# Performance work log

Measured on AMD Instinct MI355X. Metric: run time of the kernel, lower is better.

The kernel has to match this reference:

```python
import jax, jax.numpy as jnp
import numpy as np

M, L, P, KK = 8, 3, 12, 9  # n_heads, n_levels, n_points, patch_size**2

def lrelu(v):
    return jnp.where(v >= 0, v, 0.1 * v)

def conv2d(x, w, b, pad):
    y = jax.lax.conv_general_dilated(x, w, (1, 1), [(pad, pad), (pad, pad)], dimension_numbers=('NCHW', 'OIHW', 'NCHW'))
    return y + b[None, :, None, None]

def trunk(x, w1, b1, w2, b2, w3, b3, w4, b4):
    h = lrelu(conv2d(x, w1, b1, 0))
    h = lrelu(conv2d(h, w2, b2, 1))
    h = lrelu(conv2d(h, w3, b3, 1))
    return conv2d(h, w4, b4, 0)

def grid_sample(img, gx, gy, align_corners):
    # img [N,C,H,W]; gx,gy [N,Q] normalized to [-1,1]; bilinear, zeros padding
    N, C, H, W = img.shape
    if align_corners:
        ix = (gx + 1.0) * 0.5 * (W - 1)
        iy = (gy + 1.0) * 0.5 * (H - 1)
    else:
        ix = ((gx + 1.0) * W - 1.0) * 0.5
        iy = ((gy + 1.0) * H - 1.0) * 0.5
    ix0 = jnp.floor(ix); iy0 = jnp.floor(iy)
    wx1 = ix - ix0; wy1 = iy - iy0
    flat = img.reshape(N, C, H * W)
    def gather(xi, yi, wgt):
        valid = (xi >= 0) & (xi <= W - 1) & (yi >= 0) & (yi <= H - 1)
        idx = (jnp.clip(yi, 0, H - 1) * W + jnp.clip(xi, 0, W - 1)).astype(jnp.int32)
        v = jnp.take_along_axis(flat, idx[:, None, :], axis=2)
        return v * (wgt * valid)[:, None, :]
    return (gather(ix0, iy0, (1 - wx1) * (1 - wy1)) + gather(ix0 + 1, iy0, wx1 * (1 - wy1))
            + gather(ix0, iy0 + 1, (1 - wx1) * wy1) + gather(ix0 + 1, iy0 + 1, wx1 * wy1))

def flow_warp(img, flow):
    # img [n,c,h,w]; flow [n,2,h,w] in pixels; torch grid_sample align_corners=True, zeros padding
    n, c, h, w = img.shape
    gy, gx = jnp.meshgrid(jnp.arange(h, dtype=img.dtype), jnp.arange(w, dtype=img.dtype), indexing='ij')
    gxn = 2.0 * (gx[None] + flow[:, 0]) / max(w - 1, 1) - 1.0
    gyn = 2.0 * (gy[None] + flow[:, 1]) / max(h - 1, 1) - 1.0
    return grid_sample(img, gxn.reshape(n, -1), gyn.reshape(n, -1), True).reshape(n, c, h, w)

def msdeform_attn(value, loc, attn, h, w):
    # pytorch MSDeformAttn core: value [N,L*HW,M,D]; loc [N,HW,M,L,Pt,2]; attn [N,HW,M,L,Pt]
    N, _, _, D = value.shape
    HW = h * w
    Pt = loc.shape[4]
    grids = 2.0 * loc - 1.0
    sampled = []
    for l in range(L):
        v = value[:, l * HW:(l + 1) * HW].transpose(0, 2, 3, 1).reshape(N * M, D, h, w)
        g = grids[:, :, :, l].transpose(0, 2, 1, 3, 4).reshape(N * M, HW * Pt, 2)
        s = grid_sample(v, g[..., 0], g[..., 1], False)  # [N*M, D, HW*Pt]
        sampled.append(s.reshape(N * M, D, HW, Pt))
    sampled = jnp.concatenate(sampled, axis=-1)  # [N*M, D, HW, L*Pt]
    aw = attn.transpose(0, 2, 1, 3, 4).reshape(N * M, HW, L * Pt)
    out = jnp.einsum('ndqp,nqp->nqd', sampled, aw)
    return out.reshape(N, M, HW, D).transpose(0, 2, 1, 3).reshape(N, HW, M * D)

def _forward(x, flow_1, flow_2, flip_flow_1, flip_flow_2, aw_w1, aw_b1, aw_w2, aw_b2, aw_w3, aw_b3, aw_w4, aw_b4, so_w1, so_b1, so_w2, so_b2, so_w3, so_b3, so_w4, so_b4, po_w1, po_b1, po_w2, po_b2, po_w3, po_b3, po_w4, po_b4, vp_w, vp_b, op_w1, op_b1, op_w2, op_b2):
    n, t, c, h, w = x.shape
    HW = h * w
    flow_cn1 = flow_1
    flow_cn2 = flow_1 + flow_warp(flow_2, flow_cn1)
    warp1 = flow_warp(x[:, 1], flow_cn1)
    warp2 = flow_warp(x[:, 2], flow_cn2)
    extra = jnp.concatenate([x[:, 0], warp1, warp2, flow_cn1, flow_cn2], axis=1)  # [n, 3c+4, h, w]
    value = conv2d(x.reshape(n, t * c, h, w), vp_w, vp_b, 0)
    off = trunk(extra, so_w1, so_b1, so_w2, so_b2, so_w3, so_b3, so_w4, so_b4)
    aw = trunk(extra, aw_w1, aw_b1, aw_w2, aw_b2, aw_w3, aw_b3, aw_w4, aw_b4)
    po = trunk(extra, po_w1, po_b1, po_w2, po_b2, po_w3, po_b3, po_w4, po_b4)
    value = value.reshape(n, t, c, HW).transpose(0, 1, 3, 2).reshape(n, t * HW, M, c // M)
    off = off.reshape(n, -1, HW).transpose(0, 2, 1).reshape(n, HW, M, L, P, 2)
    po = po.reshape(n, -1, HW).transpose(0, 2, 1).reshape(n, HW, M, L, P)
    po = jax.nn.sigmoid(po) * 3.0
    aw = aw.reshape(n, -1, HW).transpose(0, 2, 1).reshape(n, HW, M, L * P * KK)
    aw = jax.nn.softmax(aw, axis=-1).reshape(n, HW, M, L, P * KK)
    # flow-guided per-level offsets: level0 zeros, level1 flow_cn1, level2 flow_cn2
    f1 = flow_cn1.reshape(n, 2, HW).transpose(0, 2, 1)
    f2 = flow_cn2.reshape(n, 2, HW).transpose(0, 2, 1)
    fstack = jnp.stack([jnp.zeros_like(f1), f1, f2], axis=2)  # [n,HW,L,2]
    off = off + fstack[:, :, None, :, None, :]
    # 3x3 patch around each sampling point, scaled by learned patch offsets
    a = jnp.arange(-1, 2, dtype=x.dtype)
    pnx, pny = jnp.meshgrid(a, a, indexing='ij')
    p_n = jnp.stack([pnx, pny], axis=-1).reshape(KK, 2)
    off = off[..., None, :] + p_n * po[..., None, None]  # [n,HW,M,L,P,KK,2]
    off = off.reshape(n, HW, M, L, P * KK, 2)
    # reference points (valid ratios == 1)
    ry = (jnp.arange(h, dtype=x.dtype) + 0.5) / h
    rx = (jnp.arange(w, dtype=x.dtype) + 0.5) / w
    gy, gx = jnp.meshgrid(ry, rx, indexing='ij')
    ref = jnp.stack([gx, gy], axis=-1).reshape(1, HW, 1, 1, 1, 2)
    norm = jnp.array([w, h], dtype=x.dtype)
    loc = ref + off / norm
    out = msdeform_attn(value, loc, aw, h, w)  # [n, HW, c]
    feat = out.reshape(n, h, w, c).transpose(0, 3, 1, 2)
    res = conv2d(lrelu(conv2d(feat, op_w1, op_b1, 0)), op_w2, op_b2, 0)
    return res + x[:, 0]

def setup_inputs():
    key = jax.random.key(0)
    keys = jax.random.split(key, 64)
    it = iter(range(64))
    def nrm(shape, scale):
        return jax.random.normal(keys[next(it)], shape, jnp.float32) * scale
    n, t, c, h, w = 1, 3, 64, 64, 64
    Cin = t * c + 4  # 196
    d = {}
    d['x'] = nrm((n, t, c, h, w), 1.0)
    for nm in ['flow_1', 'flow_2', 'flip_flow_1', 'flip_flow_2']:
        d[nm] = nrm((n, 2, h, w), 1.5)
    def branch(prefix, out_ch, final_scale):
        d[prefix + '_w1'] = nrm((64, Cin, 1, 1), 1.0 / np.sqrt(Cin))
        d[prefix + '_b1'] = nrm((64,), 0.01)
        d[prefix + '_w2'] = nrm((64, 64, 3, 3), 1.0 / np.sqrt(64 * 9))
        d[prefix + '_b2'] = nrm((64,), 0.01)
        d[prefix + '_w3'] = nrm((64, 64, 3, 3), 1.0 / np.sqrt(64 * 9))
        d[prefix + '_b3'] = nrm((64,), 0.01)
        d[prefix + '_w4'] = nrm((out_ch, 64, 1, 1), final_scale)
        d[prefix + '_b4'] = nrm((out_ch,), 0.01)
    branch('aw', M * L * P * KK, 0.01)
    branch('so', M * L * P * 2, 0.01)
    branch('po', M * L * P, 0.01)
    d['vp_w'] = nrm((t * c, t * c, 1, 1), 1.0 / np.sqrt(t * c))
    d['vp_b'] = nrm((t * c,), 0.01)
    d['op_w1'] = nrm((c, c, 1, 1), 1.0 / np.sqrt(c))
    d['op_b1'] = nrm((c,), 0.01)
    d['op_w2'] = nrm((c, c, 1, 1), 1.0 / np.sqrt(c))
    d['op_b2'] = nrm((c,), 0.01)
    return d

def reference(x, flow_1, flow_2, flip_flow_1, flip_flow_2, aw_w1, aw_b1, aw_w2, aw_b2, aw_w3, aw_b3, aw_w4, aw_b4, so_w1, so_b1, so_w2, so_b2, so_w3, so_b3, so_w4, so_b4, po_w1, po_b1, po_w2, po_b2, po_w3, po_b3, po_w4, po_b4, vp_w, vp_b, op_w1, op_b1, op_w2, op_b2):
    return _forward(x, flow_1, flow_2, flip_flow_1, flip_flow_2, aw_w1, aw_b1, aw_w2, aw_b2, aw_w3, aw_b3, aw_w4, aw_b4, so_w1, so_b1, so_w2, so_b2, so_w3, so_b3, so_w4, so_b4, po_w1, po_b1, po_w2, po_b2, po_w3, po_b3, po_w4, po_b4, vp_w, vp_b, op_w1, op_b1, op_w2, op_b2)
```

## Files before the change

kernel.cpp:

```cpp
#include <hip/hip_runtime.h>
#include <hip/hip_bf16.h>
#include <math.h>

#define HWN 4096

typedef __attribute__((ext_vector_type(8))) short short8;
typedef __attribute__((ext_vector_type(4))) float f32x4;

__device__ __forceinline__ float lrelu_f(float v) { return v >= 0.f ? v : 0.1f * v; }

__device__ __forceinline__ unsigned short f2bf(float f) {
  union { float f; unsigned u; } v; v.f = f;
  unsigned r = v.u + 0x7fff + ((v.u >> 16) & 1);
  return (unsigned short)(r >> 16);
}
__device__ __forceinline__ float bf2f(unsigned short u) {
  union { unsigned u; float f; } v; v.u = ((unsigned)u) << 16;
  return v.f;
}
__device__ __forceinline__ float bf_lo(unsigned u) {
  union { unsigned u; float f; } v; v.u = u << 16; return v.f;
}
__device__ __forceinline__ float bf_hi(unsigned u) {
  union { unsigned u; float f; } v; v.u = u & 0xffff0000u; return v.f;
}

__device__ __forceinline__ float bilin_zero(const float* __restrict__ img, float ix, float iy) {
  float fx0 = floorf(ix), fy0 = floorf(iy);
  int x0 = (int)fx0, y0 = (int)fy0;
  float wx1 = ix - fx0, wy1 = iy - fy0;
  float wx0 = 1.f - wx1, wy0 = 1.f - wy1;
  float acc = 0.f;
  if ((unsigned)y0 < 64u) {
    if ((unsigned)x0 < 64u)       acc += wx0 * wy0 * img[y0 * 64 + x0];
    if ((unsigned)(x0 + 1) < 64u) acc += wx1 * wy0 * img[y0 * 64 + x0 + 1];
  }
  if ((unsigned)(y0 + 1) < 64u) {
    if ((unsigned)x0 < 64u)       acc += wx0 * wy1 * img[(y0 + 1) * 64 + x0];
    if ((unsigned)(x0 + 1) < 64u) acc += wx1 * wy1 * img[(y0 + 1) * 64 + x0 + 1];
  }
  return acc;
}

__global__ void k_pre(
    const float* __restrict__ x, const float* __restrict__ flow1, const float* __restrict__ flow2,
    const float* so_w4, const float* po_w4, const float* aw_w4,
    const float* so_b4, const float* po_b4, const float* aw_b4,
    const float* so_b1, const float* po_b1, const float* aw_b1,
    const float* so_b2, const float* po_b2, const float* aw_b2,
    const float* so_b3, const float* po_b3, const float* aw_b3,
    const float* so_w1, const float* po_w1, const float* aw_w1,
    const float* so_w2, const float* po_w2, const float* aw_w2,
    const float* so_w3, const float* po_w3, const float* aw_w3,
    const float* op_w1, const float* op_w2, const float* vp_w,
    unsigned short* Wtail, float* btail, float* b1c, float* b2c, float* b3c,
    unsigned short* o1b, unsigned short* o2b, unsigned short* W1,
    unsigned short* W2g, unsigned short* W3g, unsigned short* vpb,
    unsigned short* xb, float* fcn2) {
  __shared__ unsigned short tile[64 * 65];
  int gx = blockIdx.x;
  int tid = threadIdx.x;
  if (gx < 5184) {
    int y = gx / 864;
    int t = (gx % 864) * 256 + tid;
    if (y == 0) {
      if (t < 3456 * 64) {
        int row = t >> 6, k = t & 63;
        float v = row < 576 ? so_w4[row * 64 + k]
                : row < 864 ? po_w4[(row - 576) * 64 + k]
                            : aw_w4[(row - 864) * 64 + k];
        Wtail[t] = f2bf(v);
      }
    } else if (y == 1) {
      if (t < 3456) {
        btail[t] = t < 576 ? so_b4[t] : t < 864 ? po_b4[t - 576] : aw_b4[t - 864];
      } else if (t < 3648) {
        int i = t - 3456; b1c[i] = i < 64 ? so_b1[i] : i < 128 ? po_b1[i - 64] : aw_b1[i - 128];
      } else if (t < 3840) {
        int i = t - 3648; b2c[i] = i < 64 ? so_b2[i] : i < 128 ? po_b2[i - 64] : aw_b2[i - 128];
      } else if (t < 4032) {
        int i = t - 3840; b3c[i] = i < 64 ? so_b3[i] : i < 128 ? po_b3[i - 64] : aw_b3[i - 128];
      } else if (t < 8128) {
        o1b[t - 4032] = f2bf(op_w1[t - 4032]);
      } else if (t < 12224) {
        o2b[t - 8128] = f2bf(op_w2[t - 8128]);
      }
    } else if (y == 2) {
      if (t < 192 * 224) {
        int row = t / 224, k = t % 224;
        int tr = row >> 6, lco = row & 63;
        const float* s = tr == 0 ? so_w1 : tr == 1 ? po_w1 : aw_w1;
        W1[t] = (k < 196) ? f2bf(s[lco * 196 + k]) : (unsigned short)0;
      }
    } else if (y == 3 || y == 4) {
      if (t < 3 * 64 * 576) {
        int tr = t / 36864, rem = t % 36864;
        int co = rem / 576, r2 = rem % 576;
        int kidx = r2 >> 6, ci = r2 & 63;
        const float* s;
        if (y == 3) s = tr == 0 ? so_w2 : tr == 1 ? po_w2 : aw_w2;
        else        s = tr == 0 ? so_w3 : tr == 1 ? po_w3 : aw_w3;
        (y == 3 ? W2g : W3g)[t] = f2bf(s[co * 576 + ci * 9 + kidx]);
      }
    } else {
      if (t < 192 * 192) vpb[t] = f2bf(vp_w[t]);
    }
  } else if (gx < 5376) {
    int b = gx - 5184;
    int ptile = b & 63, cg = b >> 6;
    int px = tid & 63, ch0 = (tid >> 6) * 16;
#pragma unroll
    for (int i = 0; i < 16; i++) {
      float v = x[(size_t)(cg * 64 + ch0 + i) * HWN + ptile * 64 + px];
      tile[(ch0 + i) * 65 + px] = f2bf(v);
    }
    __syncthreads();
    int c = tid & 63, pl0 = (tid >> 6) * 16;
#pragma unroll
    for (int i = 0; i < 16; i++)
      xb[(size_t)(ptile * 64 + pl0 + i) * 192 + cg * 64 + c] = tile[c * 65 + pl0 + i];
  } else {
    int p = (gx - 5376) * 256 + tid;
    int px = p & 63, py = p >> 6;
    float fx = flow1[p], fy = flow1[HWN + p];
    float ix = (float)px + fx, iy = (float)py + fy;
    fcn2[p] = fx + bilin_zero(flow2, ix, iy);
    fcn2[HWN + p] = fy + bilin_zero(flow2 + HWN, ix, iy);
  }
}

__global__ void k_extra(const unsigned short* __restrict__ xb, const float* __restrict__ flow1,
                        const float* __restrict__ fcn2, unsigned short* __restrict__ extra) {
  int w = threadIdx.x >> 6, c = threadIdx.x & 63;
  int p = blockIdx.x * 4 + w;
  int px = p & 63, py = p >> 6;
  float fx1 = flow1[p], fy1 = flow1[HWN + p];
  float fx2 = fcn2[p],  fy2 = fcn2[HWN + p];
  extra[(size_t)p * 224 + c] = xb[(size_t)p * 192 + c];
#pragma unroll
  for (int lev = 0; lev < 2; lev++) {
    float ix = (float)px + (lev ? fx2 : fx1);
    float iy = (float)py + (lev ? fy2 : fy1);
    float fx0 = floorf(ix), fy0 = floorf(iy);
    int x0 = (int)fx0, y0 = (int)fy0;
    float wx1 = ix - fx0, wy1 = iy - fy0;
    float wx0 = 1.f - wx1, wy0 = 1.f - wy1;
    int coff = (lev + 1) * 64;
    float acc = 0.f;
    if ((unsigned)y0 < 64u) {
      if ((unsigned)x0 < 64u)       acc += wx0 * wy0 * bf2f(xb[(size_t)(y0 * 64 + x0) * 192 + coff + c]);
      if ((unsigned)(x0 + 1) < 64u) acc += wx1 * wy0 * bf2f(xb[(size_t)(y0 * 64 + x0 + 1) * 192 + coff + c]);
    }
    if ((unsigned)(y0 + 1) < 64u) {
      if ((unsigned)x0 < 64u)       acc += wx0 * wy1 * bf2f(xb[(size_t)((y0 + 1) * 64 + x0) * 192 + coff + c]);
      if ((unsigned)(x0 + 1) < 64u) acc += wx1 * wy1 * bf2f(xb[(size_t)((y0 + 1) * 64 + x0 + 1) * 192 + coff + c]);
    }
    extra[(size_t)p * 224 + coff + c] = f2bf(acc);
  }
  if (c < 2) {
    extra[(size_t)p * 224 + 192 + c] = f2bf(flow1[c * HWN + p]);
    extra[(size_t)p * 224 + 194 + c] = f2bf(fcn2[c * HWN + p]);
  }
  if (c < 28) extra[(size_t)p * 224 + 196 + c] = 0;
}

__global__ __launch_bounds__(128) void k_gemm2(
    const unsigned short* __restrict__ A0, const unsigned short* __restrict__ Wm0,
    const float* __restrict__ bias0, unsigned short* __restrict__ out0,
    const unsigned short* __restrict__ A1, const unsigned short* __restrict__ Wm1,
    const float* __restrict__ bias1, unsigned short* __restrict__ out1) {
  int z = blockIdx.z;
  const unsigned short* A = z ? A1 : A0;
  const unsigned short* Wm = z ? Wm1 : Wm0;
  const float* bias = z ? bias1 : bias0;
  unsigned short* out = z ? out1 : out0;
  int K = z ? 224 : 192;

  int wv = threadIdx.x >> 6;
  int l = threadIdx.x & 63;
  int lm = l & 15, lq = l >> 4;
  int p0 = blockIdx.x * 32 + wv * 16;
  int co0 = blockIdx.y * 32;

  f32x4 acc[2];
#pragma unroll
  for (int nt = 0; nt < 2; nt++) {
    float bv = bias[co0 + nt * 16 + lm];
    acc[nt] = (f32x4){bv, bv, bv, bv};
  }
  const unsigned short* ap = A + (size_t)(p0 + lm) * K + lq * 8;
  const unsigned short* wp = Wm + (size_t)(co0 + lm) * K + lq * 8;
  for (int k0 = 0; k0 < K; k0 += 32) {
    short8 af = *(const short8*)(ap + k0);
#pragma unroll
    for (int nt = 0; nt < 2; nt++) {
      short8 bf = *(const short8*)(wp + (size_t)nt * 16 * K + k0);
      acc[nt] = __builtin_amdgcn_mfma_f32_16x16x32_bf16(af, bf, acc[nt], 0, 0, 0);
    }
  }
#pragma unroll
  for (int nt = 0; nt < 2; nt++) {
    int co = co0 + nt * 16 + lm;
#pragma unroll
    for (int r = 0; r < 4; r++) {
      int p = p0 + lq * 4 + r;
      float v = acc[nt][r];
      if (z) v = lrelu_f(v);
      out[(size_t)p * 192 + co] = f2bf(v);
    }
  }
}

__global__ __launch_bounds__(128) void k_conv3g(const unsigned short* __restrict__ h,
                                                const unsigned short* __restrict__ Wm,
                                                const float* __restrict__ bias,
                                                unsigned short* __restrict__ out) {
  int wv = threadIdx.x >> 6;
  int l = threadIdx.x & 63;
  int lm = l & 15, lq = l >> 4;
  int p0 = blockIdx.x * 32 + wv * 16;
  int co0 = blockIdx.y * 16;
  int t = blockIdx.z;
  int p = p0 + lm;
  int px = p & 63, py = p >> 6;

  float bv = bias[t * 64 + co0 + lm];
  f32x4 acc = (f32x4){bv, bv, bv, bv};
  const unsigned short* wp = Wm + ((size_t)t * 64 + co0 + lm) * 576 + lq * 8;
#pragma unroll
  for (int kidx = 0; kidx < 9; kidx++) {
    int ky = kidx / 3, kx = kidx % 3;
    int pp = p + (ky - 1) * 64 + (kx - 1);
    bool valid = ((unsigned)(px + kx - 1) < 64u) && ((unsigned)(py + ky - 1) < 64u);
    const unsigned short* apb = h + (size_t)pp * 192 + t * 64 + lq * 8;
#pragma unroll
    for (int c2 = 0; c2 < 2; c2++) {
      short8 af = {};
      if (valid) af = *(const short8*)(apb + c2 * 32);
      short8 bf = *(const short8*)(wp + kidx * 64 + c2 * 32);
      acc = __builtin_amdgcn_mfma_f32_16x16x32_bf16(af, bf, acc, 0, 0, 0);
    }
  }
#pragma unroll
  for (int r = 0; r < 4; r++) {
    int po_ = p0 + lq * 4 + r;
    out[(size_t)po_ * 192 + t * 64 + co0 + lm] = f2bf(lrelu_f(acc[r]));
  }
}

__global__ __launch_bounds__(256) void k_tail(const unsigned short* __restrict__ A,
                                              const unsigned short* __restrict__ Wm,
                                              const float* __restrict__ bias,
                                              unsigned short* __restrict__ out) {
  int wv = threadIdx.x >> 6;
  int l = threadIdx.x & 63;
  int lm = l & 15, lq = l >> 4;
  int p0 = blockIdx.x * 64 + wv * 16;
  int co0 = blockIdx.y * 32;
  int t = (co0 < 576) ? 0 : (co0 < 864 ? 1 : 2);

  f32x4 acc[2];
#pragma unroll
  for (int nt = 0; nt < 2; nt++) {
    float bv = bias[co0 + nt * 16 + lm];
    acc[nt] = (f32x4){bv, bv, bv, bv};
  }
  const unsigned short* ap = A + (size_t)(p0 + lm) * 192 + t * 64 + lq * 8;
  const unsigned short* wp = Wm + (size_t)(co0 + lm) * 64 + lq * 8;
#pragma unroll
  for (int k0 = 0; k0 < 64; k0 += 32) {
    short8 af = *(const short8*)(ap + k0);
#pragma unroll
    for (int nt = 0; nt < 2; nt++) {
      short8 bf = *(const short8*)(wp + (size_t)nt * 16 * 64 + k0);
      acc[nt] = __builtin_amdgcn_mfma_f32_16x16x32_bf16(af, bf, acc[nt], 0, 0, 0);
    }
  }
#pragma unroll
  for (int nt = 0; nt < 2; nt++) {
    int co = co0 + nt * 16 + lm;
#pragma unroll
    for (int r = 0; r < 4; r++) {
      int p = p0 + lq * 4 + r;
      float v = acc[nt][r];
      if (t == 2) v = __expf(v);
      else if (t == 1) v = 3.f * __builtin_amdgcn_rcpf(1.f + __expf(-v));
      out[(size_t)p * 3456 + co] = f2bf(v);
    }
  }
}

__global__ void k_msdeform(const unsigned short* __restrict__ vsb,
                           const unsigned short* __restrict__ to,
                           const float* __restrict__ flow1, const float* __restrict__ fcn2,
                           unsigned short* __restrict__ featb) {
  int yl = threadIdx.x & 15;
  int p = blockIdx.x * 16 + (threadIdx.x >> 4);
  int m = blockIdx.y;
  int px = p & 63, py = p >> 6;

  float fx1 = flow1[p], fy1 = flow1[HWN + p];
  float fx2 = fcn2[p],  fy2 = fcn2[HWN + p];

  const unsigned short* row = to + (size_t)p * 3456;

  float acc[8];
#pragma unroll
  for (int d = 0; d < 8; d++) acc[d] = 0.f;
  float wsum = 0.f;

  for (int pair = yl; pair < 36; pair += 16) {
    int l = pair / 12, pt = pair % 12;
    float fx = (l == 1) ? fx1 : ((l == 2) ? fx2 : 0.f);
    float fy = (l == 1) ? fy1 : ((l == 2) ? fy2 : 0.f);
    int ch = (m * 3 + l) * 12 + pt;
    unsigned ow = *(const unsigned*)(row + ch * 2);
    float ox = bf_lo(ow);
    float oy = bf_hi(ow);
    float s = bf2f(row[576 + ch]);
    float bx = (float)px + ox + fx;
    float by = (float)py + oy + fy;
    const unsigned short* vbase = vsb + l * 64 + m * 8;
    const unsigned short* lgp = row + 864 + m * 324 + l * 108 + pt * 9;
#pragma unroll
    for (int kk = 0; kk < 9; kk++) {
      float pnx = (float)(kk / 3 - 1);
      float pny = (float)(kk % 3 - 1);
      float ix = bx + pnx * s;
      float iy = by + pny * s;
      float wgt = bf2f(lgp[kk]);
      wsum += wgt;

      float fx0 = floorf(ix), fy0 = floorf(iy);
      int x0 = (int)fx0, y0 = (int)fy0;
      float wx1 = ix - fx0, wy1 = iy - fy0;
      float wx0 = 1.f - wx1, wy0 = 1.f - wy1;

      float tw[4];
      int tx[4], ty[4];
      tw[0] = wx0 * wy0; tx[0] = x0;     ty[0] = y0;
      tw[1] = wx1 * wy0; tx[1] = x0 + 1; ty[1] = y0;
      tw[2] = wx0 * wy1; tx[2] = x0;     ty[2] = y0 + 1;
      tw[3] = wx1 * wy1; tx[3] = x0 + 1; ty[3] = y0 + 1;
#pragma unroll
      for (int c = 0; c < 4; c++) {
        if ((unsigned)tx[c] < 64u && (unsigned)ty[c] < 64u) {
          uint4 uv = *(const uint4*)(vbase + (size_t)(ty[c] * 64 + tx[c]) * 192);
          float ww = wgt * tw[c];
          acc[0] += ww * bf_lo(uv.x); acc[1] += ww * bf_hi(uv.x);
          acc[2] += ww * bf_lo(uv.y); acc[3] += ww * bf_hi(uv.y);
          acc[4] += ww * bf_lo(uv.z); acc[5] += ww * bf_hi(uv.z);
          acc[6] += ww * bf_lo(uv.w); acc[7] += ww * bf_hi(uv.w);
        }
      }
    }
  }
#pragma unroll
  for (int mask = 1; mask < 16; mask <<= 1) {
    wsum += __shfl_xor(wsum, mask);
#pragma unroll
    for (int d = 0; d < 8; d++) acc[d] += __shfl_xor(acc[d], mask);
  }
  if (yl < 8) {
    float inv = __builtin_amdgcn_rcpf(wsum);
    float r = 0.f;
#pragma unroll
    for (int d = 0; d < 8; d++) r = (d == yl) ? acc[d] : r;
    featb[(size_t)p * 64 + m * 8 + yl] = f2bf(r * inv);
  }
}

__global__ __launch_bounds__(256) void k_opout(const unsigned short* __restrict__ featb,
                                               const unsigned short* __restrict__ o1b,
                                               const float* __restrict__ bias1,
                                               const unsigned short* __restrict__ o2b,
                                               const float* __restrict__ bias2,
                                               const float* __restrict__ x,
                                               float* __restrict__ out) {
  __shared__ unsigned short hop[64 * 72];
  int wv = threadIdx.x >> 6;
  int l = threadIdx.x & 63;
  int lm = l & 15, lq = l >> 4;
  int bp0 = blockIdx.x * 64;

  f32x4 acc1[4];
#pragma unroll
  for (int nt = 0; nt < 4; nt++) {
    float bv = bias1[nt * 16 + lm];
    acc1[nt] = (f32x4){bv, bv, bv, bv};
  }
  const unsigned short* ap = featb + (size_t)(bp0 + wv * 16 + lm) * 64 + lq * 8;
#pragma unroll
  for (int k0 = 0; k0 < 64; k0 += 32) {
    short8 af = *(const short8*)(ap + k0);
#pragma unroll
    for (int nt = 0; nt < 4; nt++) {
      short8 bf = *(const short8*)(o1b + (size_t)(nt * 16 + lm) * 64 + lq * 8 + k0);
      acc1[nt] = __builtin_amdgcn_mfma_f32_16x16x32_bf16(af, bf, acc1[nt], 0, 0, 0);
    }
  }
#pragma unroll
  for (int nt = 0; nt < 4; nt++)
#pragma unroll
    for (int r = 0; r < 4; r++)
      hop[(wv * 16 + lq * 4 + r) * 72 + nt * 16 + lm] = f2bf(lrelu_f(acc1[nt][r]));
  __syncthreads();

  f32x4 b4;
#pragma unroll
  for (int r = 0; r < 4; r++) b4[r] = bias2[wv * 16 + lq * 4 + r];
  f32x4 acc2[4];
#pragma unroll
  for (int pg = 0; pg < 4; pg++) acc2[pg] = b4;
#pragma unroll
  for (int k0 = 0; k0 < 64; k0 += 32) {
    short8 af = *(const short8*)(o2b + (size_t)(wv * 16 + lm) * 64 + k0 + lq * 8);
#pragma unroll
    for (int pg = 0; pg < 4; pg++) {
      short8 bf = *(const short8*)(hop + (pg * 16 + lm) * 72 + k0 + lq * 8);
      acc2[pg] = __builtin_amdgcn_mfma_f32_16x16x32_bf16(af, bf, acc2[pg], 0, 0, 0);
    }
  }
#pragma unroll
  for (int pg = 0; pg < 4; pg++) {
#pragma unroll
    for (int r = 0; r < 4; r++) {
      int co = wv * 16 + lq * 4 + r;
      int p = bp0 + pg * 16 + lm;
      out[(size_t)co * HWN + p] = acc2[pg][r] + x[(size_t)co * HWN + p];
    }
  }
}

extern "C" void kernel_launch(void* const* d_in, const int* in_sizes, int n_in,
                              void* d_out, int out_size, void* d_ws, size_t ws_size,
                              hipStream_t stream) {
  const float* x     = (const float*)d_in[0];
  const float* flow1 = (const float*)d_in[1];
  const float* flow2 = (const float*)d_in[2];
  const float* aw_w1 = (const float*)d_in[5];
  const float* aw_b1 = (const float*)d_in[6];
  const float* aw_w2 = (const float*)d_in[7];
  const float* aw_b2 = (const float*)d_in[8];
  const float* aw_w3 = (const float*)d_in[9];
  const float* aw_b3 = (const float*)d_in[10];
  const float* aw_w4 = (const float*)d_in[11];
  const float* aw_b4 = (const float*)d_in[12];
  const float* so_w1 = (const float*)d_in[13];
  const float* so_b1 = (const float*)d_in[14];
  const float* so_w2 = (const float*)d_in[15];
  const float* so_b2 = (const float*)d_in[16];
  const float* so_w3 = (const float*)d_in[17];
  const float* so_b3 = (const float*)d_in[18];
  const float* so_w4 = (const float*)d_in[19];
  const float* so_b4 = (const float*)d_in[20];
  const float* po_w1 = (const float*)d_in[21];
  const float* po_b1 = (const float*)d_in[22];
  const float* po_w2 = (const float*)d_in[23];
  const float* po_b2 = (const float*)d_in[24];
  const float* po_w3 = (const float*)d_in[25];
  const float* po_b3 = (const float*)d_in[26];
  const float* po_w4 = (const float*)d_in[27];
  const float* po_b4 = (const float*)d_in[28];
  const float* vp_w  = (const float*)d_in[29];
  const float* vp_b  = (const float*)d_in[30];
  const float* op_w1 = (const float*)d_in[31];
  const float* op_b1 = (const float*)d_in[32];
  const float* op_w2 = (const float*)d_in[33];
  const float* op_b2 = (const float*)d_in[34];

  char* base = (char*)d_ws;
  size_t off = 0;
  auto alloc = [&](size_t bytes) { void* pp = base + off; off = (off + bytes + 255) & ~(size_t)255; return pp; };

  float* fcn2  = (float*)alloc(2 * HWN * 4);
  unsigned short* xb    = (unsigned short*)alloc(192 * HWN * 2);
  unsigned short* vsb   = (unsigned short*)alloc(192 * HWN * 2);
  unsigned short* extra = (unsigned short*)alloc(224 * HWN * 2);
  unsigned short* h1    = (unsigned short*)alloc(192 * HWN * 2);
  unsigned short* h2    = (unsigned short*)alloc(192 * HWN * 2);
  unsigned short* h3    = (unsigned short*)alloc(192 * HWN * 2);
  unsigned short* to    = (unsigned short*)alloc((size_t)3456 * HWN * 2);
  unsigned short* featb = (unsigned short*)alloc(64 * HWN * 2);
  unsigned short* Wtail = (unsigned short*)alloc(3456 * 64 * 2);
  float* btail = (float*)alloc(3456 * 4);
  float* b1c   = (float*)alloc(192 * 4);
  float* b2c   = (float*)alloc(192 * 4);
  float* b3c   = (float*)alloc(192 * 4);
  unsigned short* o1b = (unsigned short*)alloc(64 * 64 * 2);
  unsigned short* o2b = (unsigned short*)alloc(64 * 64 * 2);
  unsigned short* W1  = (unsigned short*)alloc(192 * 224 * 2);
  unsigned short* W2g = (unsigned short*)alloc(3 * 64 * 576 * 2);
  unsigned short* W3g = (unsigned short*)alloc(3 * 64 * 576 * 2);
  unsigned short* vpb = (unsigned short*)alloc(192 * 192 * 2);

  k_pre<<<5392, 256, 0, stream>>>(
      x, flow1, flow2,
      so_w4, po_w4, aw_w4, so_b4, po_b4, aw_b4,
      so_b1, po_b1, aw_b1, so_b2, po_b2, aw_b2, so_b3, po_b3, aw_b3,
      so_w1, po_w1, aw_w1, so_w2, po_w2, aw_w2, so_w3, po_w3, aw_w3,
      op_w1, op_w2, vp_w,
      Wtail, btail, b1c, b2c, b3c, o1b, o2b, W1, W2g, W3g, vpb, xb, fcn2);

  k_extra<<<1024, 256, 0, stream>>>(xb, flow1, fcn2, extra);

  k_gemm2<<<dim3(128, 6, 2), 128, 0, stream>>>(xb, vpb, vp_b, vsb, extra, W1, b1c, h1);

  k_conv3g<<<dim3(128, 4, 3), 128, 0, stream>>>(h1, W2g, b2c, h2);
  k_conv3g<<<dim3(128, 4, 3), 128, 0, stream>>>(h2, W3g, b3c, h3);
  k_tail<<<dim3(64, 108), 256, 0, stream>>>(h3, Wtail, btail, to);

  k_msdeform<<<dim3(256, 8), 256, 0, stream>>>(vsb, to, flow1, fcn2, featb);

  k_opout<<<64, 256, 0, stream>>>(featb, o1b, op_b1, o2b, op_b2, x, (float*)d_out);
}
```

Baseline: 239.2 us.

## Build padded row-pair value layout so each bilinear tap loads contiguously without bounds checks

Value features are repacked into two zero-padded buffers, split by row parity, with the two vertically adjacent rows interleaved. Each bilinear sample then reads the four corner vectors as four contiguous 16-byte loads, with no per-corner bounds branches. The repack runs as extra blocks appended to k_tail, and the padding is zeroed in k_pre. The weight transpose in k_pre is also reworked to stage each weight row in shared memory and shrink the grid. This costs extra workspace and an extra copy of the value tensor, and it clamps coordinates to a two-pixel pad.

```diff
diff --git a/kernel.cpp b/kernel.cpp
--- a/kernel.cpp
+++ b/kernel.cpp
@@ -3,6 +3,9 @@
 #include <math.h>
 
 #define HWN 4096
+#define VROW 72
+#define VYP 36
+#define VSZ_SH (24 * VYP * VROW * 16)
 
 typedef __attribute__((ext_vector_type(8))) short short8;
 typedef __attribute__((ext_vector_type(4))) float f32x4;
@@ -56,57 +59,61 @@
     unsigned short* Wtail, float* btail, float* b1c, float* b2c, float* b3c,
     unsigned short* o1b, unsigned short* o2b, unsigned short* W1,
     unsigned short* W2g, unsigned short* W3g, unsigned short* vpb,
-    unsigned short* xb, float* fcn2) {
+    unsigned short* xb, float* fcn2, unsigned short* vA) {
   __shared__ unsigned short tile[64 * 65];
+  __shared__ unsigned short wrow[576];
   int gx = blockIdx.x;
   int tid = threadIdx.x;
-  if (gx < 5184) {
-    int y = gx / 864;
-    int t = (gx % 864) * 256 + tid;
-    if (y == 0) {
-      if (t < 3456 * 64) {
-        int row = t >> 6, k = t & 63;
-        float v = row < 576 ? so_w4[row * 64 + k]
-                : row < 864 ? po_w4[(row - 576) * 64 + k]
-                            : aw_w4[(row - 864) * 64 + k];
-        Wtail[t] = f2bf(v);
-      }
-    } else if (y == 1) {
-      if (t < 3456) {
-        btail[t] = t < 576 ? so_b4[t] : t < 864 ? po_b4[t - 576] : aw_b4[t - 864];
-      } else if (t < 3648) {
-        int i = t - 3456; b1c[i] = i < 64 ? so_b1[i] : i < 128 ? po_b1[i - 64] : aw_b1[i - 128];
-      } else if (t < 3840) {
-        int i = t - 3648; b2c[i] = i < 64 ? so_b2[i] : i < 128 ? po_b2[i - 64] : aw_b2[i - 128];
-      } else if (t < 4032) {
-        int i = t - 3840; b3c[i] = i < 64 ? so_b3[i] : i < 128 ? po_b3[i - 64] : aw_b3[i - 128];
-      } else if (t < 8128) {
-        o1b[t - 4032] = f2bf(op_w1[t - 4032]);
-      } else if (t < 12224) {
-        o2b[t - 8128] = f2bf(op_w2[t - 8128]);
-      }
-    } else if (y == 2) {
-      if (t < 192 * 224) {
-        int row = t / 224, k = t % 224;
-        int tr = row >> 6, lco = row & 63;
-        const float* s = tr == 0 ? so_w1 : tr == 1 ? po_w1 : aw_w1;
-        W1[t] = (k < 196) ? f2bf(s[lco * 196 + k]) : (unsigned short)0;
-      }
-    } else if (y == 3 || y == 4) {
-      if (t < 3 * 64 * 576) {
-        int tr = t / 36864, rem = t % 36864;
-        int co = rem / 576, r2 = rem % 576;
-        int kidx = r2 >> 6, ci = r2 & 63;
-        const float* s;
-        if (y == 3) s = tr == 0 ? so_w2 : tr == 1 ? po_w2 : aw_w2;
-        else        s = tr == 0 ? so_w3 : tr == 1 ? po_w3 : aw_w3;
-        (y == 3 ? W2g : W3g)[t] = f2bf(s[co * 576 + ci * 9 + kidx]);
-      }
-    } else {
-      if (t < 192 * 192) vpb[t] = f2bf(vp_w[t]);
-    }
-  } else if (gx < 5376) {
-    int b = gx - 5184;
+  if (gx < 864) {
+    int t = gx * 256 + tid;
+    int row = t >> 6, k = t & 63;
+    float v = row < 576 ? so_w4[row * 64 + k]
+            : row < 864 ? po_w4[(row - 576) * 64 + k]
+                        : aw_w4[(row - 864) * 64 + k];
+    Wtail[t] = f2bf(v);
+  } else if (gx < 912) {
+    int t = (gx - 864) * 256 + tid;
+    if (t < 3456) {
+      btail[t] = t < 576 ? so_b4[t] : t < 864 ? po_b4[t - 576] : aw_b4[t - 864];
+    } else if (t < 3648) {
+      int i = t - 3456; b1c[i] = i < 64 ? so_b1[i] : i < 128 ? po_b1[i - 64] : aw_b1[i - 128];
+    } else if (t < 3840) {
+      int i = t - 3648; b2c[i] = i < 64 ? so_b2[i] : i < 128 ? po_b2[i - 64] : aw_b2[i - 128];
+    } else if (t < 4032) {
+      int i = t - 3840; b3c[i] = i < 64 ? so_b3[i] : i < 128 ? po_b3[i - 64] : aw_b3[i - 128];
+    } else if (t < 8128) {
+      o1b[t - 4032] = f2bf(op_w1[t - 4032]);
+    } else if (t < 12224) {
+      o2b[t - 8128] = f2bf(op_w2[t - 8128]);
+    }
+  } else if (gx < 1080) {
+    int t = (gx - 912) * 256 + tid;
+    if (t < 192 * 224) {
+      int row = t / 224, k = t % 224;
+      int tr = row >> 6, lco = row & 63;
+      const float* s = tr == 0 ? so_w1 : tr == 1 ? po_w1 : aw_w1;
+      W1[t] = (k < 196) ? f2bf(s[lco * 196 + k]) : (unsigned short)0;
+    }
+  } else if (gx < 1464) {
+    int b = gx - 1080;
+    int which = b >= 192;
+    b &= 191;
+    int tr = b >> 6, co = b & 63;
+    const float* s;
+    if (!which) s = tr == 0 ? so_w2 : tr == 1 ? po_w2 : aw_w2;
+    else        s = tr == 0 ? so_w3 : tr == 1 ? po_w3 : aw_w3;
+    unsigned short* d = which ? W3g : W2g;
+#pragma unroll
+    for (int j = tid; j < 576; j += 256) wrow[j] = f2bf(s[co * 576 + j]);
+    __syncthreads();
+#pragma unroll
+    for (int j = tid; j < 576; j += 256)
+      d[((size_t)tr * 64 + co) * 576 + j] = wrow[(j & 63) * 9 + (j >> 6)];
+  } else if (gx < 1608) {
+    int t = (gx - 1464) * 256 + tid;
+    if (t < 192 * 192) vpb[t] = f2bf(vp_w[t]);
+  } else if (gx < 1800) {
+    int b = gx - 1608;
     int ptile = b & 63, cg = b >> 6;
     int px = tid & 63, ch0 = (tid >> 6) * 16;
 #pragma unroll
@@ -119,13 +126,16 @@
 #pragma unroll
     for (int i = 0; i < 16; i++)
       xb[(size_t)(ptile * 64 + pl0 + i) * 192 + cg * 64 + c] = tile[c * 65 + pl0 + i];
-  } else {
-    int p = (gx - 5376) * 256 + tid;
+  } else if (gx < 1816) {
+    int p = (gx - 1800) * 256 + tid;
     int px = p & 63, py = p >> 6;
     float fx = flow1[p], fy = flow1[HWN + p];
     float ix = (float)px + fx, iy = (float)py + fy;
     fcn2[p] = fx + bilin_zero(flow2, ix, iy);
     fcn2[HWN + p] = fy + bilin_zero(flow2 + HWN, ix, iy);
+  } else {
+    int i = (gx - 1816) * 256 + tid;
+    if (i < 2 * VSZ_SH / 8) ((uint4*)vA)[i] = make_uint4(0, 0, 0, 0);
   }
 }
 
@@ -251,7 +261,21 @@
 __global__ __launch_bounds__(256) void k_tail(const unsigned short* __restrict__ A,
                                               const unsigned short* __restrict__ Wm,
                                               const float* __restrict__ bias,
-                                              unsigned short* __restrict__ out) {
+                                              unsigned short* __restrict__ out,
+                                              const unsigned short* __restrict__ vsb,
+                                              unsigned short* __restrict__ vA,
+                                              unsigned short* __restrict__ vB) {
+  if (blockIdx.y >= 108) {
+    int i = ((blockIdx.y - 108) * 64 + blockIdx.x) * 256 + threadIdx.x;
+    int lm = i % 24, p = i / 24;
+    uint4 v = ((const uint4*)vsb)[p * 24 + lm];
+    int y = p >> 6, xx = p & 63;
+    int ypA = (y >> 1) + 1, slotA = y & 1;
+    int ypB = (y + 1) >> 1, slotB = (y & 1) ^ 1;
+    ((uint4*)vA)[((lm * VYP + ypA) * VROW + xx + 2) * 2 + slotA] = v;
+    ((uint4*)vB)[((lm * VYP + ypB) * VROW + xx + 2) * 2 + slotB] = v;
+    return;
+  }
   int wv = threadIdx.x >> 6;
   int l = threadIdx.x & 63;
   int lm = l & 15, lq = l >> 4;
@@ -290,7 +314,8 @@
   }
 }
 
-__global__ void k_msdeform(const unsigned short* __restrict__ vsb,
+__global__ void k_msdeform(const unsigned short* __restrict__ vA,
+                           const unsigned short* __restrict__ vB,
                            const unsigned short* __restrict__ to,
                            const float* __restrict__ flow1, const float* __restrict__ fcn2,
                            unsigned short* __restrict__ featb) {
@@ -310,18 +335,19 @@
   float wsum = 0.f;
 
   for (int pair = yl; pair < 36; pair += 16) {
-    int l = pair / 12, pt = pair % 12;
-    float fx = (l == 1) ? fx1 : ((l == 2) ? fx2 : 0.f);
-    float fy = (l == 1) ? fy1 : ((l == 2) ? fy2 : 0.f);
-    int ch = (m * 3 + l) * 12 + pt;
+    int lv = pair / 12, pt = pair % 12;
+    float fx = (lv == 1) ? fx1 : ((lv == 2) ? fx2 : 0.f);
+    float fy = (lv == 1) ? fy1 : ((lv == 2) ? fy2 : 0.f);
+    int ch = (m * 3 + lv) * 12 + pt;
     unsigned ow = *(const unsigned*)(row + ch * 2);
     float ox = bf_lo(ow);
     float oy = bf_hi(ow);
     float s = bf2f(row[576 + ch]);
     float bx = (float)px + ox + fx;
     float by = (float)py + oy + fy;
-    const unsigned short* vbase = vsb + l * 64 + m * 8;
-    const unsigned short* lgp = row + 864 + m * 324 + l * 108 + pt * 9;
+    int lmz = lv * 8 + m;
+    int lmoff = lmz * (VYP * VROW * 16);
+    const unsigned short* lgp = row + 864 + m * 324 + lv * 108 + pt * 9;
 #pragma unroll
     for (int kk = 0; kk < 9; kk++) {
       float pnx = (float)(kk / 3 - 1);
@@ -332,27 +358,31 @@
       wsum += wgt;
 
       float fx0 = floorf(ix), fy0 = floorf(iy);
-      int x0 = (int)fx0, y0 = (int)fy0;
       float wx1 = ix - fx0, wy1 = iy - fy0;
       float wx0 = 1.f - wx1, wy0 = 1.f - wy1;
-
-      float tw[4];
-      int tx[4], ty[4];
-      tw[0] = wx0 * wy0; tx[0] = x0;     ty[0] = y0;
-      tw[1] = wx1 * wy0; tx[1] = x0 + 1; ty[1] = y0;
-      tw[2] = wx0 * wy1; tx[2] = x0;     ty[2] = y0 + 1;
-      tw[3] = wx1 * wy1; tx[3] = x0 + 1; ty[3] = y0 + 1;
-#pragma unroll
-      for (int c = 0; c < 4; c++) {
-        if ((unsigned)tx[c] < 64u && (unsigned)ty[c] < 64u) {
-          uint4 uv = *(const uint4*)(vbase + (size_t)(ty[c] * 64 + tx[c]) * 192);
-          float ww = wgt * tw[c];
-          acc[0] += ww * bf_lo(uv.x); acc[1] += ww * bf_hi(uv.x);
-          acc[2] += ww * bf_lo(uv.y); acc[3] += ww * bf_hi(uv.y);
-          acc[4] += ww * bf_lo(uv.z); acc[5] += ww * bf_hi(uv.z);
-          acc[6] += ww * bf_lo(uv.w); acc[7] += ww * bf_hi(uv.w);
-        }
-      }
+      int x0 = min(max((int)fx0, -2), 66);
+      int y0 = min(max((int)fy0, -2), 66);
+      int par = y0 & 1;
+      int yp = (y0 + 2 - par) >> 1;
+      const unsigned short* vb = par ? vB : vA;
+      int idx = lmoff + (yp * VROW + x0 + 2) * 16;
+
+      uint4 q0 = *(const uint4*)(vb + idx);
+      uint4 q1 = *(const uint4*)(vb + idx + 8);
+      uint4 q2 = *(const uint4*)(vb + idx + 16);
+      uint4 q3 = *(const uint4*)(vb + idx + 24);
+
+      float w00 = wgt * wx0 * wy0, w01 = wgt * wx0 * wy1;
+      float w10 = wgt * wx1 * wy0, w11 = wgt * wx1 * wy1;
+
+      acc[0] += w00 * bf_lo(q0.x) + w01 * bf_lo(q1.x) + w10 * bf_lo(q2.x) + w11 * bf_lo(q3.x);
+      acc[1] += w00 * bf_hi(q0.x) + w01 * bf_hi(q1.x) + w10 * bf_hi(q2.x) + w11 * bf_hi(q3.x);
+      acc[2] += w00 * bf_lo(q0.y) + w01 * bf_lo(q1.y) + w10 * bf_lo(q2.y) + w11 * bf_lo(q3.y);
+      acc[3] += w00 * bf_hi(q0.y) + w01 * bf_hi(q1.y) + w10 * bf_hi(q2.y) + w11 * bf_hi(q3.y);
+      acc[4] += w00 * bf_lo(q0.z) + w01 * bf_lo(q1.z) + w10 * bf_lo(q2.z) + w11 * bf_lo(q3.z);
+      acc[5] += w00 * bf_hi(q0.z) + w01 * bf_hi(q1.z) + w10 * bf_hi(q2.z) + w11 * bf_hi(q3.z);
+      acc[6] += w00 * bf_lo(q0.w) + w01 * bf_lo(q1.w) + w10 * bf_lo(q2.w) + w11 * bf_lo(q3.w);
+      acc[7] += w00 * bf_hi(q0.w) + w01 * bf_hi(q1.w) + w10 * bf_hi(q2.w) + w11 * bf_hi(q3.w);
     }
   }
 #pragma unroll
@@ -482,6 +512,8 @@
   unsigned short* h3    = (unsigned short*)alloc(192 * HWN * 2);
   unsigned short* to    = (unsigned short*)alloc((size_t)3456 * HWN * 2);
   unsigned short* featb = (unsigned short*)alloc(64 * HWN * 2);
+  unsigned short* vA    = (unsigned short*)alloc((size_t)VSZ_SH * 2 * 2);
+  unsigned short* vB    = vA + VSZ_SH;
   unsigned short* Wtail = (unsigned short*)alloc(3456 * 64 * 2);
   float* btail = (float*)alloc(3456 * 4);
   float* b1c   = (float*)alloc(192 * 4);
@@ -494,13 +526,13 @@
   unsigned short* W3g = (unsigned short*)alloc(3 * 64 * 576 * 2);
   unsigned short* vpb = (unsigned short*)alloc(192 * 192 * 2);
 
-  k_pre<<<5392, 256, 0, stream>>>(
+  k_pre<<<2788, 256, 0, stream>>>(
       x, flow1, flow2,
       so_w4, po_w4, aw_w4, so_b4, po_b4, aw_b4,
       so_b1, po_b1, aw_b1, so_b2, po_b2, aw_b2, so_b3, po_b3, aw_b3,
       so_w1, po_w1, aw_w1, so_w2, po_w2, aw_w2, so_w3, po_w3, aw_w3,
       op_w1, op_w2, vp_w,
-      Wtail, btail, b1c, b2c, b3c, o1b, o2b, W1, W2g, W3g, vpb, xb, fcn2);
+      Wtail, btail, b1c, b2c, b3c, o1b, o2b, W1, W2g, W3g, vpb, xb, fcn2, vA);
 
   k_extra<<<1024, 256, 0, stream>>>(xb, flow1, fcn2, extra);
 
@@ -508,9 +540,9 @@
 
   k_conv3g<<<dim3(128, 4, 3), 128, 0, stream>>>(h1, W2g, b2c, h2);
   k_conv3g<<<dim3(128, 4, 3), 128, 0, stream>>>(h2, W3g, b3c, h3);
-  k_tail<<<dim3(64, 108), 256, 0, stream>>>(h3, Wtail, btail, to);
-
-  k_msdeform<<<dim3(256, 8), 256, 0, stream>>>(vsb, to, flow1, fcn2, featb);
+  k_tail<<<dim3(64, 114), 256, 0, stream>>>(h3, Wtail, btail, to, vsb, vA, vB);
+
+  k_msdeform<<<dim3(256, 8), 256, 0, stream>>>(vA, vB, to, flow1, fcn2, featb);
 
   k_opout<<<64, 256, 0, stream>>>(featb, o1b, op_b1, o2b, op_b2, x, (float*)d_out);
 }
```

After: 627.1 us. 162% more time.
